# Kernel optimization log

Hardware: AMD Instinct MI355X
Metric: run time of the kernel (lower is better)

## Reference

```python
import jax, jax.numpy as jnp
import numpy as np

B, N, DIM, PDIM, K = 2, 4096, 512, 64, 16
ALPHA, SIGMA = 0.1, 1.0


def setup_inputs() -> dict:
    key = jax.random.key(0)
    ks = jax.random.split(key, 6)
    sf = 1.0 / np.sqrt(DIM)
    return {
        "states": jax.random.normal(ks[0], (B, N, DIM), jnp.float32),
        "positions": jax.random.normal(ks[1], (B, N, PDIM), jnp.float32),
        "W_flow": jax.random.uniform(ks[2], (PDIM, DIM), jnp.float32, -sf, sf),
        "b_flow": jax.random.uniform(ks[3], (PDIM,), jnp.float32, -sf, sf),
        "W_val": jax.random.uniform(ks[4], (DIM, DIM), jnp.float32, -sf, sf),
        "b_val": jax.random.uniform(ks[5], (DIM,), jnp.float32, -sf, sf),
    }


def _pairwise_dist(p):
    sq = jnp.sum(p * p, axis=-1)  # [B,N]
    d2 = sq[:, :, None] + sq[:, None, :] - 2.0 * jnp.einsum('bnp,bmp->bnm', p, p)
    return jnp.sqrt(jnp.maximum(d2, 1e-12))


def reference(states, positions, W_flow, b_flow, W_val, b_val):
    # flow projection + position update
    flow = jnp.einsum('bnd,pd->bnp', states, W_flow) + b_flow  # [B,N,PDIM]
    new_pos = positions + ALPHA * flow

    # kNN search (exclude self via large diagonal)
    d = _pairwise_dist(new_pos)  # [B,N,N]
    d_knn = d + jnp.eye(N, dtype=d.dtype) * 1e6
    _, nbrs = jax.lax.top_k(-d_knn, K)  # [B,N,K] smallest distances

    # scatter neighbor mask [B,N,N] (no [B,N,K,N] one-hot materialization)
    bidx = jnp.arange(B)[:, None, None]
    ridx = jnp.arange(N)[None, :, None]
    mask = jnp.zeros((B, N, N), d.dtype).at[bidx, ridx, nbrs].set(1.0)

    # gaussian affinities; exp(-d*mask)*mask == exp(-d)*mask on the support
    aff = jnp.exp(-d / (2.0 * SIGMA ** 2)) * mask
    aff = aff / (jnp.sum(aff, axis=-1, keepdims=True) + 1e-8)

    # value projection + weighted aggregation
    values = jnp.einsum('bnd,ed->bne', states, W_val) + b_val  # [B,N,DIM]
    context = jnp.einsum('bnm,bmd->bnd', aff, values)
    return context, new_pos, flow
```

## Files before the change

### kernel.cpp

```cpp
#include <hip/hip_runtime.h>

#define NB 2
#define NN 4096
#define DIMD 512
#define PD 64
#define KNN 16
#define QB 8
#define CAP 192
#define CTRIG 52
#define RCAP 48
#define MROWS (NB*NN)
#define FLOW_BLOCKS (MROWS/4)

typedef unsigned short ushort_t;

__global__ __launch_bounds__(256)
void prep_kernel(const float* __restrict__ states, const float* __restrict__ positions,
                 const float* __restrict__ W_flow, const float* __restrict__ b_flow,
                 const float* __restrict__ W_val, const float* __restrict__ b_val,
                 float* __restrict__ out_np, float* __restrict__ out_fl,
                 float* __restrict__ npos_lo, float* __restrict__ p4t,
                 double* __restrict__ sq64, float* __restrict__ sqf,
                 float* __restrict__ values_ws)
{
    __shared__ float s_lds[4][DIMD];
    __shared__ float As[16][68];
    __shared__ float Bs[16][68];
    const int t = threadIdx.x;

    if (blockIdx.x < FLOW_BLOCKS) {
        const int row0 = blockIdx.x * 4;
        const float4* src = (const float4*)(states + (size_t)row0 * DIMD);
        float4* dst = (float4*)&s_lds[0][0];
        dst[t] = src[t];
        dst[t + 256] = src[t + 256];
        __syncthreads();
        const int lr = t >> 6;
        const int p  = t & 63;
        const int row = row0 + lr;
        const float4* wr = (const float4*)(W_flow + (size_t)p * DIMD);
        const float4* sr = (const float4*)&s_lds[lr][0];
        double a0 = 0.0, a1 = 0.0, a2 = 0.0, a3 = 0.0;
        #pragma unroll 8
        for (int d4 = 0; d4 < DIMD/4; ++d4) {
            float4 w4 = wr[d4];
            float4 s4 = sr[d4];
            a0 += (double)s4.x * (double)w4.x;
            a1 += (double)s4.y * (double)w4.y;
            a2 += (double)s4.z * (double)w4.z;
            a3 += (double)s4.w * (double)w4.w;
        }
        double acc = ((a0 + a1) + (a2 + a3)) + (double)b_flow[p];
        const size_t g = (size_t)row * PD + p;
        double np_ = (double)positions[g] + 0.1 * acc;
        float hi = (float)np_;
        float lo = (float)(np_ - (double)hi);
        out_fl[g]   = (float)acc;
        out_np[g]   = hi;
        npos_lo[g]  = lo;
        const int bb = row >> 12, n = row & (NN - 1);
        p4t[(((size_t)bb*16 + (p >> 2))*NN + n)*4 + (p & 3)] = hi;
        double s2 = np_ * np_;
        #pragma unroll
        for (int off = 32; off >= 1; off >>= 1) s2 += __shfl_xor(s2, off);
        if (p == 0) { sq64[row] = s2; sqf[row] = (float)s2; }
    } else {
        const int idx = blockIdx.x - FLOW_BLOCKS;
        const int bn = idx & 7, bm = idx >> 3;
        const int lr  = t >> 2;
        const int lc4 = (t & 3) << 2;
        const int cr = (t >> 4) << 2;
        const int cc = (t & 15) << 2;
        float acc[4][4] = {};
        for (int k0 = 0; k0 < DIMD; k0 += 16) {
            float4 av = *(const float4*)(states + (size_t)(bm*64 + lr)*DIMD + k0 + lc4);
            float4 wv = *(const float4*)(W_val  + (size_t)(bn*64 + lr)*DIMD + k0 + lc4);
            __syncthreads();
            As[lc4+0][lr] = av.x; As[lc4+1][lr] = av.y; As[lc4+2][lr] = av.z; As[lc4+3][lr] = av.w;
            Bs[lc4+0][lr] = wv.x; Bs[lc4+1][lr] = wv.y; Bs[lc4+2][lr] = wv.z; Bs[lc4+3][lr] = wv.w;
            __syncthreads();
            #pragma unroll
            for (int kk = 0; kk < 16; ++kk) {
                float4 a  = *(const float4*)&As[kk][cr];
                float4 b4 = *(const float4*)&Bs[kk][cc];
                acc[0][0] += a.x*b4.x; acc[0][1] += a.x*b4.y; acc[0][2] += a.x*b4.z; acc[0][3] += a.x*b4.w;
                acc[1][0] += a.y*b4.x; acc[1][1] += a.y*b4.y; acc[1][2] += a.y*b4.z; acc[1][3] += a.y*b4.w;
                acc[2][0] += a.z*b4.x; acc[2][1] += a.z*b4.y; acc[2][2] += a.z*b4.z; acc[2][3] += a.z*b4.w;
                acc[3][0] += a.w*b4.x; acc[3][1] += a.w*b4.y; acc[3][2] += a.w*b4.z; acc[3][3] += a.w*b4.w;
            }
        }
        const int colb = bn*64 + cc;
        float4 bb = *(const float4*)(b_val + colb);
        #pragma unroll
        for (int i = 0; i < 4; ++i) {
            float4 o;
            o.x = acc[i][0] + bb.x;
            o.y = acc[i][1] + bb.y;
            o.z = acc[i][2] + bb.z;
            o.w = acc[i][3] + bb.w;
            *(float4*)(values_ws + (size_t)(bm*64 + cr + i)*DIMD + colb) = o;
        }
    }
}

__global__ __launch_bounds__(256, 4)
void dist_kernel(const float* __restrict__ nph, const float* __restrict__ npl,
                 const float4* __restrict__ p4t, const float* __restrict__ sqf,
                 const double* __restrict__ sq64, const float* __restrict__ values,
                 float* __restrict__ ctx)
{
    __shared__ __align__(16) unsigned char POOL[24576];
    __shared__ float    qstage[QB][68];
    __shared__ ushort_t rlist[QB][4][RCAP];
    __shared__ int      ccnt[QB][4];
    __shared__ int      rcnt[QB][4];

    ushort_t (*sd16)[4][CAP]  = (ushort_t(*)[4][CAP])POOL;
    ushort_t (*six16)[4][CAP] = (ushort_t(*)[4][CAP])(POOL + 12288);
    double (*umbd)[192] = (double(*)[192])POOL;
    int*    umbi        = (int*)(POOL + 12288);
    double (*qd64)[66]  = (double(*)[66])(POOL + 18432);
    int*    fin_ix      = (int*)(POOL + 22656);
    float*  fin_w       = (float*)(POOL + 23168);

    const int tid  = threadIdx.x;
    const int w    = tid >> 6;
    const int lane = tid & 63;
    const int b    = blockIdx.x >> 9;
    const int n0   = (blockIdx.x & 511) << 3;
    const int base = b * NN;

    if (tid < 32) ccnt[tid >> 2][tid & 3] = 0;
    if (tid < 128) {
        int row = tid >> 4, c4 = (tid & 15) << 2;
        *(float4*)&qstage[row][c4] = *(const float4*)(nph + (size_t)(base + n0 + row)*PD + c4);
    }
    __syncthreads();

    float sqq[QB], tv[QB];
    #pragma unroll
    for (int j = 0; j < QB; ++j) { sqq[j] = sqf[base + n0 + j]; tv[j] = 1e30f; }

    const float4* P4 = p4t + (size_t)b * 16 * NN;
    const int qbase = w << 10;

    for (int ch = 0; ch < 8; ++ch) {
        const int cbase = qbase + (ch << 7);
        const int c0 = cbase + lane, c1 = c0 + 64;
        float a[QB][2];
        #pragma unroll
        for (int j = 0; j < QB; ++j) { a[j][0] = 0.f; a[j][1] = 0.f; }
        #pragma unroll
        for (int k4 = 0; k4 < 16; ++k4) {
            float4 p0 = P4[(size_t)k4*NN + c0];
            float4 p1 = P4[(size_t)k4*NN + c1];
            #pragma unroll
            for (int j = 0; j < QB; ++j) {
                float4 qv = *(const float4*)&qstage[j][k4 << 2];
                a[j][0] += qv.x*p0.x + qv.y*p0.y + qv.z*p0.z + qv.w*p0.w;
                a[j][1] += qv.x*p1.x + qv.y*p1.y + qv.z*p1.z + qv.w*p1.w;
            }
        }
        const float sc0 = sqf[base + c0], sc1 = sqf[base + c1];
        #pragma unroll
        for (int j = 0; j < QB; ++j) {
            float d0 = fmaxf(sqq[j] + sc0 - 2.f*a[j][0], 0.f);
            float d1 = fmaxf(sqq[j] + sc1 - 2.f*a[j][1], 0.f);
            if (c0 == n0 + j) d0 = 1e30f;
            if (c1 == n0 + j) d1 = 1e30f;
            a[j][0] = d0; a[j][1] = d1;
        }

        if (ch == 0) {
            #pragma unroll
            for (int j = 0; j < QB; ++j) {
                unsigned lo = 0u, hi = 0x7F80u;
                #pragma unroll 1
                for (int it = 0; it < 16; ++it) {
                    unsigned mid = (lo + hi) >> 1;
                    float fm = __uint_as_float(mid << 16);
                    int cnt = __popcll(__ballot(a[j][0] < fm)) + __popcll(__ballot(a[j][1] < fm));
                    if (cnt >= 19) hi = mid; else lo = mid;
                }
                tv[j] = __uint_as_float(hi << 16);
            }
        }

        #pragma unroll
        for (int j = 0; j < QB; ++j) {
            if (a[j][0] < tv[j]) {
                int s = atomicAdd(&ccnt[j][w], 1);
                if (s < CAP) {
                    sd16[j][w][s]  = (ushort_t)(__float_as_uint(a[j][0]) >> 16);
                    six16[j][w][s] = (ushort_t)c0;
                }
            }
            if (a[j][1] < tv[j]) {
                int s = atomicAdd(&ccnt[j][w], 1);
                if (s < CAP) {
                    sd16[j][w][s]  = (ushort_t)(__float_as_uint(a[j][1]) >> 16);
                    six16[j][w][s] = (ushort_t)c1;
                }
            }
        }

        #pragma unroll
        for (int j = 0; j < QB; ++j) {
            int cnt0 = ccnt[j][w];
            if (cnt0 > CTRIG) {
                if (cnt0 > CAP) cnt0 = CAP;
                ushort_t v0 = (lane       < cnt0) ? sd16[j][w][lane]       : (ushort_t)0xFFFF;
                ushort_t v1 = (64 + lane  < cnt0) ? sd16[j][w][64 + lane]  : (ushort_t)0xFFFF;
                ushort_t v2 = (128 + lane < cnt0) ? sd16[j][w][128 + lane] : (ushort_t)0xFFFF;
                ushort_t i0 = (lane       < cnt0) ? six16[j][w][lane]       : (ushort_t)0;
                ushort_t i1 = (64 + lane  < cnt0) ? six16[j][w][64 + lane]  : (ushort_t)0;
                ushort_t i2 = (128 + lane < cnt0) ? six16[j][w][128 + lane] : (ushort_t)0;
                unsigned lo = 0u, hi = 0x7F80u;
                #pragma unroll 1
                for (int it = 0; it < 16; ++it) {
                    unsigned mid = (lo + hi) >> 1;
                    int cnt = __popcll(__ballot((unsigned)v0 < mid))
                            + __popcll(__ballot((unsigned)v1 < mid))
                            + __popcll(__ballot((unsigned)v2 < mid));
                    if (cnt >= 19) hi = mid; else lo = mid;
                }
                tv[j] = __uint_as_float(hi << 16);
                if (lane == 0) ccnt[j][w] = 0;
                if ((unsigned)v0 < hi) { int s = atomicAdd(&ccnt[j][w], 1); sd16[j][w][s] = v0; six16[j][w][s] = i0; }
                if ((unsigned)v1 < hi) { int s = atomicAdd(&ccnt[j][w], 1); sd16[j][w][s] = v1; six16[j][w][s] = i1; }
                if ((unsigned)v2 < hi) { int s = atomicAdd(&ccnt[j][w], 1); sd16[j][w][s] = v2; six16[j][w][s] = i2; }
            }
        }
    }

    if (lane < QB) rcnt[lane][w] = 0;
    #pragma unroll 1
    for (int j = 0; j < QB; ++j) {
        int cnt0 = ccnt[j][w];
        if (cnt0 > CAP) cnt0 = CAP;
        ushort_t v0 = (lane       < cnt0) ? sd16[j][w][lane]       : (ushort_t)0xFFFF;
        ushort_t v1 = (64 + lane  < cnt0) ? sd16[j][w][64 + lane]  : (ushort_t)0xFFFF;
        ushort_t v2 = (128 + lane < cnt0) ? sd16[j][w][128 + lane] : (ushort_t)0xFFFF;
        ushort_t i0 = (lane       < cnt0) ? six16[j][w][lane]       : (ushort_t)0;
        ushort_t i1 = (64 + lane  < cnt0) ? six16[j][w][64 + lane]  : (ushort_t)0;
        ushort_t i2 = (128 + lane < cnt0) ? six16[j][w][128 + lane] : (ushort_t)0;
        unsigned lo = 0u, hi = 0x7F80u;
        #pragma unroll 1
        for (int it = 0; it < 16; ++it) {
            unsigned mid = (lo + hi) >> 1;
            int cnt = __popcll(__ballot((unsigned)v0 < mid))
                    + __popcll(__ballot((unsigned)v1 < mid))
                    + __popcll(__ballot((unsigned)v2 < mid));
            if (cnt >= 20) hi = mid; else lo = mid;
        }
        if ((unsigned)v0 < hi) { int s = atomicAdd(&rcnt[j][w], 1); if (s < RCAP) rlist[j][w][s] = i0; }
        if ((unsigned)v1 < hi) { int s = atomicAdd(&rcnt[j][w], 1); if (s < RCAP) rlist[j][w][s] = i1; }
        if ((unsigned)v2 < hi) { int s = atomicAdd(&rcnt[j][w], 1); if (s < RCAP) rlist[j][w][s] = i2; }
    }
    __syncthreads();

    for (int i = tid; i < QB*PD; i += 256) {
        int q = i >> 6, p = i & 63;
        size_t g = (size_t)(base + n0 + q)*PD + p;
        qd64[q][p] = (double)nph[g] + (double)npl[g];
    }
    for (int i = tid; i < QB*192; i += 256) {
        umbd[i / 192][i % 192] = 1e300;
        umbi[i] = 0x7fffffff;
    }
    __syncthreads();

    const int lh = lane & 15, g4 = lane >> 4;
    #pragma unroll 1
    for (int q = 0; q < QB; ++q) {
        int cr = rcnt[q][w]; if (cr > RCAP) cr = RCAP;
        const double qd0 = qd64[q][4*lh+0], qd1 = qd64[q][4*lh+1];
        const double qd2 = qd64[q][4*lh+2], qd3 = qd64[q][4*lh+3];
        const double sq_q = sq64[base + n0 + q];
        for (int s0 = 0; s0 < cr; s0 += 4) {
            const int slot = s0 + g4;
            const bool valid = slot < cr;
            const int cand = valid ? (int)rlist[q][w][slot] : 0;
            const float4 h4 = *(const float4*)(nph + (size_t)(base + cand)*PD + 4*lh);
            const float4 l4 = *(const float4*)(npl + (size_t)(base + cand)*PD + 4*lh);
            double acc = qd0*((double)h4.x + (double)l4.x)
                       + qd1*((double)h4.y + (double)l4.y)
                       + qd2*((double)h4.z + (double)l4.z)
                       + qd3*((double)h4.w + (double)l4.w);
            #pragma unroll
            for (int off = 1; off < 16; off <<= 1) acc += __shfl_xor(acc, off);
            if (valid && lh == 0) {
                umbd[q][w*RCAP + slot] = sq_q + sq64[base + cand] - 2.0*acc;
                umbi[q*192 + w*RCAP + slot] = cand;
            }
        }
    }
    __syncthreads();

    #pragma unroll 1
    for (int qi = 0; qi < 2; ++qi) {
        const int q = 2*w + qi;
        double ev0 = umbd[q][lane], ev1 = umbd[q][64 + lane], ev2 = umbd[q][128 + lane];
        int ei0 = umbi[q*192 + lane], ei1 = umbi[q*192 + 64 + lane], ei2 = umbi[q*192 + 128 + lane];
        double wsum = 0.0, mywk = 0.0;
        for (int r = 0; r < KNN; ++r) {
            double bv = ev0; int bi = ei0; int bs = 0;
            if (ev1 < bv || (ev1 == bv && ei1 < bi)) { bv = ev1; bi = ei1; bs = 1; }
            if (ev2 < bv || (ev2 == bv && ei2 < bi)) { bv = ev2; bi = ei2; bs = 2; }
            #pragma unroll
            for (int off = 32; off >= 1; off >>= 1) {
                double ov = __shfl_xor(bv, off);
                int    oi = __shfl_xor(bi, off);
                if (ov < bv || (ov == bv && oi < bi)) { bv = ov; bi = oi; }
            }
            if (bs == 0 && ei0 == bi) ev0 = 1e300;
            if (bs == 1 && ei1 == bi) ev1 = 1e300;
            if (bs == 2 && ei2 == bi) ev2 = 1e300;
            double wk = exp(-0.5 * sqrt(fmax(bv, 1e-12)));
            wsum += wk;
            if (lane == r) mywk = wk;
            if (lane == 0) fin_ix[q*16 + r] = bi;
        }
        if (lane < KNN) fin_w[q*16 + lane] = (float)(mywk / (wsum + 1e-8));
    }
    __syncthreads();

    {
        const int q  = tid >> 5;
        const int e0 = (tid & 31) << 4;
        const float* V = values + (size_t)base * DIMD;
        float acc2[16] = {};
        for (int k = 0; k < KNN; ++k) {
            int   m  = fin_ix[q*16 + k];
            float wg = fin_w[q*16 + k];
            const float4* vr = (const float4*)(V + (size_t)m*DIMD + e0);
            #pragma unroll
            for (int t4 = 0; t4 < 4; ++t4) {
                float4 vv = vr[t4];
                acc2[4*t4+0] += wg*vv.x; acc2[4*t4+1] += wg*vv.y;
                acc2[4*t4+2] += wg*vv.z; acc2[4*t4+3] += wg*vv.w;
            }
        }
        float* crow = ctx + (size_t)(base + n0 + q)*DIMD + e0;
        #pragma unroll
        for (int t4 = 0; t4 < 4; ++t4)
            *(float4*)(crow + 4*t4) = make_float4(acc2[4*t4+0], acc2[4*t4+1], acc2[4*t4+2], acc2[4*t4+3]);
    }
}

extern "C" void kernel_launch(void* const* d_in, const int* in_sizes, int n_in,
                              void* d_out, int out_size, void* d_ws, size_t ws_size,
                              hipStream_t stream)
{
    (void)in_sizes; (void)n_in; (void)out_size; (void)ws_size;
    const float* states    = (const float*)d_in[0];
    const float* positions = (const float*)d_in[1];
    const float* W_flow    = (const float*)d_in[2];
    const float* b_flow    = (const float*)d_in[3];
    const float* W_val     = (const float*)d_in[4];
    const float* b_val     = (const float*)d_in[5];

    float* out_ctx = (float*)d_out;
    float* out_np  = out_ctx + (size_t)NB*NN*DIMD;
    float* out_fl  = out_np  + (size_t)NB*NN*PD;

    char* ws = (char*)d_ws;
    float*  values_ws = (float*)ws;
    float*  npos_lo   = (float*)(ws + (size_t)16777216);
    double* sq64      = (double*)(ws + (size_t)18874368);
    float*  sqf       = (float*)(ws + (size_t)18939904);
    float*  p4t       = (float*)(ws + (size_t)18972672);

    hipLaunchKernelGGL(prep_kernel, dim3(FLOW_BLOCKS + (DIMD/64)*(MROWS/64)), dim3(256), 0, stream,
                       states, positions, W_flow, b_flow, W_val, b_val,
                       out_np, out_fl, npos_lo, p4t, sq64, sqf, values_ws);
    hipLaunchKernelGGL(dist_kernel, dim3(NB*512), dim3(256), 0, stream,
                       out_np, npos_lo, (const float4*)p4t, sqf, sq64, values_ws, out_ctx);
}
```

Baseline: 383.9 us.

## Overlap value GEMM with kNN search by splitting kernels into three stages

Moves the value projection GEMM out of the prep kernel and interleaves its blocks with the kNN distance blocks in a new middle kernel, so the GEMM runs concurrently with the neighbor search. Neighbor indices and weights are staged in the context output buffer, and a third kernel does the weighted gather. This lets the flow kernel finish sooner and fills idle compute during the search, at the cost of an extra launch and a small round trip through global memory.

New measurement: 507.9 us. +32.3%, slower.

```diff
diff --git a/kernel.cpp b/kernel.cpp
--- a/kernel.cpp
+++ b/kernel.cpp
@@ -10,67 +10,80 @@
 #define CTRIG 52
 #define RCAP 48
 #define MROWS (NB*NN)
-#define FLOW_BLOCKS (MROWS/4)
 
 typedef unsigned short ushort_t;
 
 __global__ __launch_bounds__(256)
-void prep_kernel(const float* __restrict__ states, const float* __restrict__ positions,
+void flow_kernel(const float* __restrict__ states, const float* __restrict__ positions,
                  const float* __restrict__ W_flow, const float* __restrict__ b_flow,
-                 const float* __restrict__ W_val, const float* __restrict__ b_val,
                  float* __restrict__ out_np, float* __restrict__ out_fl,
                  float* __restrict__ npos_lo, float* __restrict__ p4t,
-                 double* __restrict__ sq64, float* __restrict__ sqf,
-                 float* __restrict__ values_ws)
+                 double* __restrict__ sq64, float* __restrict__ sqf)
 {
     __shared__ float s_lds[4][DIMD];
-    __shared__ float As[16][68];
-    __shared__ float Bs[16][68];
     const int t = threadIdx.x;
-
-    if (blockIdx.x < FLOW_BLOCKS) {
-        const int row0 = blockIdx.x * 4;
-        const float4* src = (const float4*)(states + (size_t)row0 * DIMD);
-        float4* dst = (float4*)&s_lds[0][0];
-        dst[t] = src[t];
-        dst[t + 256] = src[t + 256];
-        __syncthreads();
-        const int lr = t >> 6;
-        const int p  = t & 63;
-        const int row = row0 + lr;
-        const float4* wr = (const float4*)(W_flow + (size_t)p * DIMD);
-        const float4* sr = (const float4*)&s_lds[lr][0];
-        double a0 = 0.0, a1 = 0.0, a2 = 0.0, a3 = 0.0;
-        #pragma unroll 8
-        for (int d4 = 0; d4 < DIMD/4; ++d4) {
-            float4 w4 = wr[d4];
-            float4 s4 = sr[d4];
-            a0 += (double)s4.x * (double)w4.x;
-            a1 += (double)s4.y * (double)w4.y;
-            a2 += (double)s4.z * (double)w4.z;
-            a3 += (double)s4.w * (double)w4.w;
-        }
-        double acc = ((a0 + a1) + (a2 + a3)) + (double)b_flow[p];
-        const size_t g = (size_t)row * PD + p;
-        double np_ = (double)positions[g] + 0.1 * acc;
-        float hi = (float)np_;
-        float lo = (float)(np_ - (double)hi);
-        out_fl[g]   = (float)acc;
-        out_np[g]   = hi;
-        npos_lo[g]  = lo;
-        const int bb = row >> 12, n = row & (NN - 1);
-        p4t[(((size_t)bb*16 + (p >> 2))*NN + n)*4 + (p & 3)] = hi;
-        double s2 = np_ * np_;
-        #pragma unroll
-        for (int off = 32; off >= 1; off >>= 1) s2 += __shfl_xor(s2, off);
-        if (p == 0) { sq64[row] = s2; sqf[row] = (float)s2; }
-    } else {
-        const int idx = blockIdx.x - FLOW_BLOCKS;
+    const int row0 = blockIdx.x * 4;
+    const float4* src = (const float4*)(states + (size_t)row0 * DIMD);
+    float4* dst = (float4*)&s_lds[0][0];
+    dst[t] = src[t];
+    dst[t + 256] = src[t + 256];
+    __syncthreads();
+    const int lr = t >> 6;
+    const int p  = t & 63;
+    const int row = row0 + lr;
+    const float4* wr = (const float4*)(W_flow + (size_t)p * DIMD);
+    const float4* sr = (const float4*)&s_lds[lr][0];
+    double a0 = 0.0, a1 = 0.0, a2 = 0.0, a3 = 0.0;
+    #pragma unroll 8
+    for (int d4 = 0; d4 < DIMD/4; ++d4) {
+        float4 w4 = wr[d4];
+        float4 s4 = sr[d4];
+        a0 += (double)s4.x * (double)w4.x;
+        a1 += (double)s4.y * (double)w4.y;
+        a2 += (double)s4.z * (double)w4.z;
+        a3 += (double)s4.w * (double)w4.w;
+    }
+    double acc = ((a0 + a1) + (a2 + a3)) + (double)b_flow[p];
+    const size_t g = (size_t)row * PD + p;
+    double np_ = (double)positions[g] + 0.1 * acc;
+    float hi = (float)np_;
+    float lo = (float)(np_ - (double)hi);
+    out_fl[g]   = (float)acc;
+    out_np[g]   = hi;
+    npos_lo[g]  = lo;
+    const int bb = row >> 12, n = row & (NN - 1);
+    p4t[(((size_t)bb*16 + (p >> 2))*NN + n)*4 + (p & 3)] = hi;
+    double s2 = np_ * np_;
+    #pragma unroll
+    for (int off = 32; off >= 1; off >>= 1) s2 += __shfl_xor(s2, off);
+    if (p == 0) { sq64[row] = s2; sqf[row] = (float)s2; }
+}
+
+__global__ __launch_bounds__(256, 4)
+void mid_kernel(const float* __restrict__ nph, const float* __restrict__ npl,
+                const float4* __restrict__ p4t, const float* __restrict__ sqf,
+                const double* __restrict__ sq64,
+                const float* __restrict__ states, const float* __restrict__ W_val,
+                const float* __restrict__ b_val, float* __restrict__ values_ws,
+                float* __restrict__ ctx)
+{
+    __shared__ __align__(16) unsigned char POOL[24576];
+    __shared__ float    qstage[QB][68];
+    __shared__ ushort_t rlist[QB][4][RCAP];
+    __shared__ int      ccnt[QB][4];
+    __shared__ int      rcnt[QB][4];
+
+    const int tid = threadIdx.x;
+    const int idx = blockIdx.x >> 1;
+
+    if (blockIdx.x & 1) {
+        float (*As)[68] = (float(*)[68])POOL;
+        float (*Bs)[68] = (float(*)[68])(POOL + 4352);
         const int bn = idx & 7, bm = idx >> 3;
-        const int lr  = t >> 2;
-        const int lc4 = (t & 3) << 2;
-        const int cr = (t >> 4) << 2;
-        const int cc = (t & 15) << 2;
+        const int lr  = tid >> 2;
+        const int lc4 = (tid & 3) << 2;
+        const int cr = (tid >> 4) << 2;
+        const int cc = (tid & 15) << 2;
         float acc[4][4] = {};
         for (int k0 = 0; k0 < DIMD; k0 += 16) {
             float4 av = *(const float4*)(states + (size_t)(bm*64 + lr)*DIMD + k0 + lc4);
@@ -100,20 +113,8 @@
             o.w = acc[i][3] + bb.w;
             *(float4*)(values_ws + (size_t)(bm*64 + cr + i)*DIMD + colb) = o;
         }
-    }
-}
-
-__global__ __launch_bounds__(256, 4)
-void dist_kernel(const float* __restrict__ nph, const float* __restrict__ npl,
-                 const float4* __restrict__ p4t, const float* __restrict__ sqf,
-                 const double* __restrict__ sq64, const float* __restrict__ values,
-                 float* __restrict__ ctx)
-{
-    __shared__ __align__(16) unsigned char POOL[24576];
-    __shared__ float    qstage[QB][68];
-    __shared__ ushort_t rlist[QB][4][RCAP];
-    __shared__ int      ccnt[QB][4];
-    __shared__ int      rcnt[QB][4];
+        return;
+    }
 
     ushort_t (*sd16)[4][CAP]  = (ushort_t(*)[4][CAP])POOL;
     ushort_t (*six16)[4][CAP] = (ushort_t(*)[4][CAP])(POOL + 12288);
@@ -123,11 +124,10 @@
     int*    fin_ix      = (int*)(POOL + 22656);
     float*  fin_w       = (float*)(POOL + 23168);
 
-    const int tid  = threadIdx.x;
     const int w    = tid >> 6;
     const int lane = tid & 63;
-    const int b    = blockIdx.x >> 9;
-    const int n0   = (blockIdx.x & 511) << 3;
+    const int b    = idx >> 9;
+    const int n0   = (idx & 511) << 3;
     const int base = b * NN;
 
     if (tid < 32) ccnt[tid >> 2][tid & 3] = 0;
@@ -325,27 +325,49 @@
     }
     __syncthreads();
 
-    {
-        const int q  = tid >> 5;
-        const int e0 = (tid & 31) << 4;
-        const float* V = values + (size_t)base * DIMD;
-        float acc2[16] = {};
-        for (int k = 0; k < KNN; ++k) {
-            int   m  = fin_ix[q*16 + k];
-            float wg = fin_w[q*16 + k];
-            const float4* vr = (const float4*)(V + (size_t)m*DIMD + e0);
-            #pragma unroll
-            for (int t4 = 0; t4 < 4; ++t4) {
-                float4 vv = vr[t4];
-                acc2[4*t4+0] += wg*vv.x; acc2[4*t4+1] += wg*vv.y;
-                acc2[4*t4+2] += wg*vv.z; acc2[4*t4+3] += wg*vv.w;
-            }
-        }
-        float* crow = ctx + (size_t)(base + n0 + q)*DIMD + e0;
-        #pragma unroll
-        for (int t4 = 0; t4 < 4; ++t4)
-            *(float4*)(crow + 4*t4) = make_float4(acc2[4*t4+0], acc2[4*t4+1], acc2[4*t4+2], acc2[4*t4+3]);
-    }
+    if (tid < 128) {
+        int q = tid >> 4, k = tid & 15;
+        size_t r = (size_t)(base + n0 + q) * DIMD;
+        ((int*)ctx)[r + k] = fin_ix[q*16 + k];
+        ctx[r + 16 + k]    = fin_w[q*16 + k];
+    }
+}
+
+__global__ __launch_bounds__(256)
+void ctx_kernel(const float* __restrict__ values, float* __restrict__ ctx)
+{
+    __shared__ int   s_ix[QB][16];
+    __shared__ float s_w[QB][16];
+    const int tid = threadIdx.x;
+    const int b    = blockIdx.x >> 9;
+    const int n0   = (blockIdx.x & 511) << 3;
+    const int base = b * NN;
+    if (tid < 128) {
+        int q = tid >> 4, k = tid & 15;
+        size_t r = (size_t)(base + n0 + q) * DIMD;
+        s_ix[q][k] = ((const int*)ctx)[r + k];
+        s_w[q][k]  = ctx[r + 16 + k];
+    }
+    __syncthreads();
+    const int q  = tid >> 5;
+    const int e0 = (tid & 31) << 4;
+    const float* V = values + (size_t)base * DIMD;
+    float acc2[16] = {};
+    for (int k = 0; k < KNN; ++k) {
+        int   m  = s_ix[q][k];
+        float wg = s_w[q][k];
+        const float4* vr = (const float4*)(V + (size_t)m*DIMD + e0);
+        #pragma unroll
+        for (int t4 = 0; t4 < 4; ++t4) {
+            float4 vv = vr[t4];
+            acc2[4*t4+0] += wg*vv.x; acc2[4*t4+1] += wg*vv.y;
+            acc2[4*t4+2] += wg*vv.z; acc2[4*t4+3] += wg*vv.w;
+        }
+    }
+    float* crow = ctx + (size_t)(base + n0 + q)*DIMD + e0;
+    #pragma unroll
+    for (int t4 = 0; t4 < 4; ++t4)
+        *(float4*)(crow + 4*t4) = make_float4(acc2[4*t4+0], acc2[4*t4+1], acc2[4*t4+2], acc2[4*t4+3]);
 }
 
 extern "C" void kernel_launch(void* const* d_in, const int* in_sizes, int n_in,
@@ -371,9 +393,12 @@
     float*  sqf       = (float*)(ws + (size_t)18939904);
     float*  p4t       = (float*)(ws + (size_t)18972672);
 
-    hipLaunchKernelGGL(prep_kernel, dim3(FLOW_BLOCKS + (DIMD/64)*(MROWS/64)), dim3(256), 0, stream,
-                       states, positions, W_flow, b_flow, W_val, b_val,
-                       out_np, out_fl, npos_lo, p4t, sq64, sqf, values_ws);
-    hipLaunchKernelGGL(dist_kernel, dim3(NB*512), dim3(256), 0, stream,
-                       out_np, npos_lo, (const float4*)p4t, sqf, sq64, values_ws, out_ctx);
+    hipLaunchKernelGGL(flow_kernel, dim3(MROWS/4), dim3(256), 0, stream,
+                       states, positions, W_flow, b_flow, out_np, out_fl,
+                       npos_lo, p4t, sq64, sqf);
+    hipLaunchKernelGGL(mid_kernel, dim3(2048), dim3(256), 0, stream,
+                       out_np, npos_lo, (const float4*)p4t, sqf, sq64,
+                       states, W_val, b_val, values_ws, out_ctx);
+    hipLaunchKernelGGL(ctx_kernel, dim3(1024), dim3(256), 0, stream,
+                       values_ws, out_ctx);
 }
```
